# Kernel tuning notes

Measured on AMD Instinct MI355X. Metric: run time of the kernel, lower is better.

Reference implementation:

```python
import jax, jax.numpy as jnp
import numpy as np

B, D, K, E = 4096, 2048, 512, 8  # tokens, model dim, kept SVD rank, experts


def setup_inputs() -> dict:
    key = jax.random.key(0)
    ks = jax.random.split(key, 7)
    x = jax.random.normal(ks[0], (B, D), dtype=jnp.float32)
    # frozen base weight (stands in for pretrained_weight)
    W = jax.random.normal(ks[1], (D, D), dtype=jnp.float32) / np.sqrt(D)
    # frozen truncated SVD factors: U_k (D,K) left vecs, V_k (K,D) as sliced in the torch code
    U_k = jnp.linalg.qr(jax.random.normal(ks[2], (D, K), dtype=jnp.float32))[0]
    V_k = jnp.linalg.qr(jax.random.normal(ks[3], (D, K), dtype=jnp.float32))[0].T
    lambda_k = jax.random.normal(ks[4], (E, K), dtype=jnp.float32) * 0.02
    v = jnp.zeros((D,), dtype=jnp.float32)
    router_W1 = jax.random.normal(ks[5], (K, 1), dtype=jnp.float32)
    router_W2 = jax.random.normal(ks[6], (1, E), dtype=jnp.float32)
    return {"x": x, "W": W, "U_k": U_k, "V_k": V_k, "lambda_k": lambda_k,
            "v": v, "router_W1": router_W1, "router_W2": router_W2}


def reference(x, W, U_k, V_k, lambda_k, v, router_W1, router_W2):
    # routing: x @ U_k -> rank-1 router -> softmax over experts
    routing = x @ U_k                                   # (B,K)
    g = jax.nn.softmax((routing @ router_W1) @ router_W2, axis=-1)  # (B,E)
    # per-expert low-rank delta weight, materialized as in the original
    delta_W = jnp.einsum('dk,ek,kn->edn', U_k, lambda_k, V_k)       # (E,D,D)
    W_tot = W[None] + delta_W                           # (E,D,D)
    # F.linear semantics: out = x @ W_tot^T per expert
    expert_out = jnp.einsum('bd,end->ben', x, W_tot)    # (B,E,D)
    out = jnp.einsum('ben,be->bn', expert_out, g)       # gated combine
    return out * (1.0 + v)
```

## Files before the change

kernel.cpp:

```cpp
#include <hip/hip_runtime.h>
#include <hip/hip_bf16.h>
#include <cstdint>

#define B_TOK 4096
#define DDIM  2048
#define KR    512
#define NE    8

using f32x4  = __attribute__((ext_vector_type(4))) float;
using short8 = __attribute__((ext_vector_type(8))) short;
using u16 = unsigned short;

__device__ inline u16 f2bf(float f) {
    union { float f; uint32_t u; } x; x.f = f;
    uint32_t u = x.u;
    return (u16)((u + 0x7fffu + ((u >> 16) & 1u)) >> 16);
}
__device__ inline float bf2f(u16 h) {
    union { uint32_t u; float f; } x; x.u = ((uint32_t)h) << 16;
    return x.f;
}

__device__ inline void gload_lds16(const u16* g, u16* l) {
    __builtin_amdgcn_global_load_lds(
        (const __attribute__((address_space(1))) void*)g,
        (__attribute__((address_space(3))) void*)l, 16, 0, 0);
}

template<int COLS4, int SRC_LD, int DST_LD>
__device__ inline void cvt_region(const float* __restrict__ src,
                                  u16* __restrict__ dst, int i) {
    int r = i / COLS4, c = i - r * COLS4;
    float4 val = *((const float4*)(src + (size_t)r * SRC_LD) + c);
    ushort4 o;
    o.x = f2bf(val.x); o.y = f2bf(val.y); o.z = f2bf(val.z); o.w = f2bf(val.w);
    *(ushort4*)(dst + (size_t)r * DST_LD + c * 4) = o;
}

__global__ __launch_bounds__(256)
void prep_all(const float* __restrict__ x, const float* __restrict__ W,
              const float* __restrict__ U, const float* __restrict__ V,
              const float* __restrict__ W1,
              u16* __restrict__ Aaug, u16* __restrict__ BigB,
              u16* __restrict__ Vb) {
    constexpr int NB_COPY = 1792;
    constexpr int N_X = 4096 * 512;
    constexpr int N_W = 2048 * 512;
    constexpr int N_U = 2048 * 128;
    constexpr int N_V = 512 * 512;
    constexpr int N_Z = 63 * 512;
    constexpr int N_TOT = N_X + N_W + N_U + N_V + N_Z;
    int b = blockIdx.x;
    if (b < NB_COPY) {
        for (int i = b * 256 + threadIdx.x; i < N_TOT; i += NB_COPY * 256) {
            if (i < N_X)                cvt_region<512, 2048, 2560>(x, Aaug, i);
            else if (i < N_X + N_W)     cvt_region<512, 2048, 2560>(W, BigB, i - N_X);
            else if (i < N_X + N_W + N_U)
                cvt_region<128, 512, 2560>(U, BigB + 2048, i - N_X - N_W);
            else if (i < N_X + N_W + N_U + N_V)
                cvt_region<512, 2048, 2048>(V, Vb, i - N_X - N_W - N_U);
            else {
                int z = i - (N_X + N_W + N_U + N_V);
                ushort4 zz; zz.x = 0; zz.y = 0; zz.z = 0; zz.w = 0;
                *(ushort4*)(Vb + (size_t)513 * 2048 + (size_t)z * 4) = zz;
            }
        }
    } else {
        int wrow = (b - NB_COPY) * 4 + (threadIdx.x >> 6);
        int lane = threadIdx.x & 63;
        const float* row = U + (size_t)wrow * KR;
        float s = 0.f;
        #pragma unroll
        for (int k = 0; k < KR; k += 64) s += row[k + lane] * W1[k + lane];
        #pragma unroll
        for (int o = 32; o > 0; o >>= 1) s += __shfl_down(s, o);
        if (lane == 0) Vb[(size_t)512 * 2048 + wrow] = f2bf(s);
    }
}

__global__ __launch_bounds__(256)
void router3(const u16* __restrict__ tb, const float* __restrict__ W2,
             const float* __restrict__ lam, u16* __restrict__ Am) {
    int row = blockIdx.x, tid = threadIdx.x;
    const u16* tr = tb + (size_t)row * 576;
    float s = bf2f(tr[512]);

    float g[NE]; float mx = -1e30f;
    #pragma unroll
    for (int e = 0; e < NE; e++) { g[e] = s * W2[e]; mx = fmaxf(mx, g[e]); }
    float den = 0.f;
    #pragma unroll
    for (int e = 0; e < NE; e++) { g[e] = expf(g[e] - mx); den += g[e]; }
    float inv = 1.0f / den;

    #pragma unroll
    for (int kk = tid; kk < KR; kk += 256) {
        float mu = 0.f;
        #pragma unroll
        for (int e = 0; e < NE; e++) mu += g[e] * lam[e * KR + kk];
        Am[(size_t)row * 2560 + 2048 + kk] = f2bf(mu * inv * bf2f(tr[kk]));
    }
}

template<int BM, int BN, int WGM, int WGN, bool HAS_V, bool OUT_BF16>
__global__ __launch_bounds__(256, 2)
void gemm_db(const u16* __restrict__ A, const u16* __restrict__ Bm,
             void* __restrict__ Cv, const float* __restrict__ v,
             int N, int Kc, int lda, int ldb, int nbx) {
    constexpr int MF = BM / (WGM * 16);
    constexpr int NF = BN / (WGN * 16);
    constexpr int ISSA = BM / 32;
    constexpr int ISSB = BN / 32;
    __shared__ u16 sA[2 * BM * 64];
    __shared__ u16 sB[2 * BN * 64];

    const int tid = threadIdx.x;
    const int wid = tid >> 6, lane = tid & 63;
    const int l15 = lane & 15, l4 = lane >> 4;
    const int wm = wid / WGN, wn = wid % WGN;

    const int nwg = gridDim.x;
    const int id = (blockIdx.x & 7) * (nwg >> 3) + (blockIdx.x >> 3);
    const int row0 = (id / nbx) * BM;
    const int col0 = (id % nbx) * BN;

    const int srow = tid >> 3;
    const int scol = ((tid & 7) ^ (srow & 7)) << 3;
    const u16* gA = A + (size_t)(row0 + srow) * lda + scol;
    const u16* gB = Bm + (size_t)(col0 + srow) * ldb + scol;

    f32x4 acc[MF][NF] = {};
    const int nt = Kc >> 6;

    #pragma unroll
    for (int i = 0; i < ISSA; i++)
        gload_lds16(gA + (size_t)i * 32 * lda, sA + i * 2048 + wid * 512);
    #pragma unroll
    for (int i = 0; i < ISSB; i++)
        gload_lds16(gB + (size_t)i * 32 * ldb, sB + i * 2048 + wid * 512);
    __syncthreads();

    for (int t = 0; t < nt; ++t) {
        const int cur = t & 1;
        if (t + 1 < nt) {
            const int nxt = cur ^ 1;
            const u16* gAk = gA + (size_t)(t + 1) * 64;
            const u16* gBk = gB + (size_t)(t + 1) * 64;
            #pragma unroll
            for (int i = 0; i < ISSA; i++)
                gload_lds16(gAk + (size_t)i * 32 * lda,
                            sA + nxt * BM * 64 + i * 2048 + wid * 512);
            #pragma unroll
            for (int i = 0; i < ISSB; i++)
                gload_lds16(gBk + (size_t)i * 32 * ldb,
                            sB + nxt * BN * 64 + i * 2048 + wid * 512);
        }
        const u16* a0 = sA + cur * BM * 64;
        const u16* b0 = sB + cur * BN * 64;
        #pragma unroll
        for (int kc = 0; kc < 8; kc += 4) {
            short8 af[MF], bv[NF];
            #pragma unroll
            for (int mf = 0; mf < MF; mf++) {
                int row = wm * MF * 16 + mf * 16 + l15;
                int ch = (kc + l4) ^ (row & 7);
                af[mf] = *(const short8*)(a0 + row * 64 + ch * 8);
            }
            #pragma unroll
            for (int nf = 0; nf < NF; nf++) {
                int row = wn * NF * 16 + nf * 16 + l15;
                int ch = (kc + l4) ^ (row & 7);
                bv[nf] = *(const short8*)(b0 + row * 64 + ch * 8);
            }
            #pragma unroll
            for (int mf = 0; mf < MF; mf++)
                #pragma unroll
                for (int nf = 0; nf < NF; nf++)
                    acc[mf][nf] = __builtin_amdgcn_mfma_f32_16x16x32_bf16(
                        af[mf], bv[nf], acc[mf][nf], 0, 0, 0);
        }
        __syncthreads();
    }

    #pragma unroll
    for (int nf = 0; nf < NF; nf++) {
        int col = col0 + wn * NF * 16 + nf * 16 + l15;
        float sc = HAS_V ? (1.0f + v[col]) : 1.0f;
        #pragma unroll
        for (int mf = 0; mf < MF; mf++) {
            int row = row0 + wm * MF * 16 + mf * 16 + l4 * 4;
            #pragma unroll
            for (int r2 = 0; r2 < 4; r2++) {
                float val = acc[mf][nf][r2] * sc;
                if constexpr (OUT_BF16)
                    ((u16*)Cv)[(size_t)(row + r2) * N + col] = f2bf(val);
                else
                    ((float*)Cv)[(size_t)(row + r2) * N + col] = val;
            }
        }
    }
}

template<bool HAS_V, bool REGION>
__global__ __launch_bounds__(512, 1)
void gemm_ring(const u16* __restrict__ A, const u16* __restrict__ Bm,
               float* __restrict__ C, const float* __restrict__ v,
               int N, int Kc, int lda, int ldb, int nbx) {
    constexpr int BM = 256, BN = 128, WGN = 2;
    constexpr int MF = 4, NF = 4;
    constexpr int SLOT = (BM + BN) * 64;
    constexpr int ROWS = 64;
    constexpr int ISSA = 4, ISSB = 2;
    __shared__ u16 lds[3 * SLOT];

    const int tid = threadIdx.x;
    const int wid = tid >> 6, lane = tid & 63;
    const int l15 = lane & 15, l4 = lane >> 4;
    const int wm = wid / WGN, wn = wid % WGN;

    int row0, col0;
    if (REGION) {
        const int xcd = blockIdx.x & 7;
        const int j = blockIdx.x >> 3;
        row0 = ((xcd >> 1) * 4 + (j >> 3)) * BM;
        col0 = ((xcd & 1) * 8 + (j & 7)) * BN;
    } else {
        const int nwg = gridDim.x;
        const int id = (blockIdx.x & 7) * (nwg >> 3) + (blockIdx.x >> 3);
        row0 = (id / nbx) * BM;
        col0 = (id % nbx) * BN;
    }

    const int srow = tid >> 3;
    const int scol = ((tid & 7) ^ (srow & 7)) << 3;
    const u16* gA = A + (size_t)(row0 + srow) * lda + scol;
    const u16* gB = Bm + (size_t)(col0 + srow) * ldb + scol;

    f32x4 acc[MF][NF] = {};
    const int nt = Kc >> 6;

    #pragma unroll
    for (int p = 0; p < 2; p++) {
        const u16* gAt = gA + p * 64;
        const u16* gBt = gB + p * 64;
        u16* sl = lds + p * SLOT;
        #pragma unroll
        for (int i = 0; i < ISSA; i++)
            gload_lds16(gAt + (size_t)i * ROWS * lda,
                        sl + i * ROWS * 64 + wid * 512);
        #pragma unroll
        for (int i = 0; i < ISSB; i++)
            gload_lds16(gBt + (size_t)i * ROWS * ldb,
                        sl + BM * 64 + i * ROWS * 64 + wid * 512);
    }
    asm volatile("s_waitcnt vmcnt(6)" ::: "memory");
    __builtin_amdgcn_s_barrier();
    asm volatile("" ::: "memory");

    int sc = 0, sp = 2;
    for (int t = 0; t < nt; ++t) {
        if (t + 2 < nt) {
            const u16* gAt = gA + (size_t)(t + 2) * 64;
            const u16* gBt = gB + (size_t)(t + 2) * 64;
            u16* sl = lds + sp * SLOT;
            #pragma unroll
            for (int i = 0; i < ISSA; i++)
                gload_lds16(gAt + (size_t)i * ROWS * lda,
                            sl + i * ROWS * 64 + wid * 512);
            #pragma unroll
            for (int i = 0; i < ISSB; i++)
                gload_lds16(gBt + (size_t)i * ROWS * ldb,
                            sl + BM * 64 + i * ROWS * 64 + wid * 512);
        }
        const u16* a0 = lds + sc * SLOT;
        const u16* b0 = a0 + BM * 64;
        __builtin_amdgcn_s_setprio(1);
        #pragma unroll
        for (int kc = 0; kc < 8; kc += 4) {
            short8 af[MF], bv[NF];
            #pragma unroll
            for (int mf = 0; mf < MF; mf++) {
                int row = wm * MF * 16 + mf * 16 + l15;
                int ch = (kc + l4) ^ (row & 7);
                af[mf] = *(const short8*)(a0 + row * 64 + ch * 8);
            }
            #pragma unroll
            for (int nf = 0; nf < NF; nf++) {
                int row = wn * NF * 16 + nf * 16 + l15;
                int ch = (kc + l4) ^ (row & 7);
                bv[nf] = *(const short8*)(b0 + row * 64 + ch * 8);
            }
            #pragma unroll
            for (int mf = 0; mf < MF; mf++)
                #pragma unroll
                for (int nf = 0; nf < NF; nf++)
                    acc[mf][nf] = __builtin_amdgcn_mfma_f32_16x16x32_bf16(
                        af[mf], bv[nf], acc[mf][nf], 0, 0, 0);
        }
        __builtin_amdgcn_s_setprio(0);

        const int rem = nt - 1 - t;
        if (rem == 0) break;
        if (rem >= 2) asm volatile("s_waitcnt vmcnt(6)" ::: "memory");
        else          asm volatile("s_waitcnt vmcnt(0)" ::: "memory");
        __builtin_amdgcn_s_barrier();
        asm volatile("" ::: "memory");
        sc = (sc == 2) ? 0 : sc + 1;
        sp = (sp == 2) ? 0 : sp + 1;
    }

    #pragma unroll
    for (int nf = 0; nf < NF; nf++) {
        int col = col0 + wn * NF * 16 + nf * 16 + l15;
        float sc2 = HAS_V ? (1.0f + v[col]) : 1.0f;
        #pragma unroll
        for (int mf = 0; mf < MF; mf++) {
            int row = row0 + wm * MF * 16 + mf * 16 + l4 * 4;
            #pragma unroll
            for (int r2 = 0; r2 < 4; r2++)
                C[(size_t)(row + r2) * N + col] = acc[mf][nf][r2] * sc2;
        }
    }
}

extern "C" void kernel_launch(void* const* d_in, const int* in_sizes, int n_in,
                              void* d_out, int out_size, void* d_ws, size_t ws_size,
                              hipStream_t stream) {
    const float* x   = (const float*)d_in[0];
    const float* W   = (const float*)d_in[1];
    const float* U   = (const float*)d_in[2];
    const float* V   = (const float*)d_in[3];
    const float* lam = (const float*)d_in[4];
    const float* v   = (const float*)d_in[5];
    const float* W1  = (const float*)d_in[6];
    const float* W2  = (const float*)d_in[7];
    float* out = (float*)d_out;

    char* ws = (char*)d_ws;
    u16* Aaug  = (u16*)ws;
    u16* BigB  = (u16*)(ws + 20971520);
    u16* Vb    = (u16*)(ws + 31457280);
    u16* tmatb = (u16*)(ws + 33816576);

    prep_all<<<2304, 256, 0, stream>>>(x, W, U, V, W1, Aaug, BigB, Vb);

    gemm_db<128, 64, 4, 1, false, true><<<288, 256, 0, stream>>>(
        Aaug, Vb, tmatb, nullptr, 576, 2048, 2560, 2048, 9);

    router3<<<4096, 256, 0, stream>>>(tmatb, W2, lam, Aaug);

    gemm_ring<true, true><<<256, 512, 0, stream>>>(
        Aaug, BigB, out, v, 2048, 2560, 2560, 2560, 16);
}
```

Baseline: 99.55 us.

## Overlap W/U bf16 conversion with routing GEMM via extra blocks; precompute LDS offsets

The fp32-to-bf16 conversion of W and U moves out of the prep kernel into 256 extra blocks appended to the routing GEMM launch, so this conversion runs alongside the small GEMM instead of serialising before it. Prep shrinks to x and V conversion with fewer blocks. The main ring GEMM also precomputes swizzled LDS offsets once per thread instead of recomputing them every k-tile. This adds register pressure in the ring kernel and relies on the extra blocks not slowing the GEMM blocks they share the device with.

```diff
diff --git a/kernel.cpp b/kernel.cpp
--- a/kernel.cpp
+++ b/kernel.cpp
@@ -38,29 +38,21 @@
 }
 
 __global__ __launch_bounds__(256)
-void prep_all(const float* __restrict__ x, const float* __restrict__ W,
-              const float* __restrict__ U, const float* __restrict__ V,
-              const float* __restrict__ W1,
-              u16* __restrict__ Aaug, u16* __restrict__ BigB,
-              u16* __restrict__ Vb) {
-    constexpr int NB_COPY = 1792;
+void prep_all(const float* __restrict__ x, const float* __restrict__ U,
+              const float* __restrict__ V, const float* __restrict__ W1,
+              u16* __restrict__ Aaug, u16* __restrict__ Vb) {
+    constexpr int NB_COPY = 1024;
     constexpr int N_X = 4096 * 512;
-    constexpr int N_W = 2048 * 512;
-    constexpr int N_U = 2048 * 128;
     constexpr int N_V = 512 * 512;
     constexpr int N_Z = 63 * 512;
-    constexpr int N_TOT = N_X + N_W + N_U + N_V + N_Z;
+    constexpr int N_TOT = N_X + N_V + N_Z;
     int b = blockIdx.x;
     if (b < NB_COPY) {
         for (int i = b * 256 + threadIdx.x; i < N_TOT; i += NB_COPY * 256) {
-            if (i < N_X)                cvt_region<512, 2048, 2560>(x, Aaug, i);
-            else if (i < N_X + N_W)     cvt_region<512, 2048, 2560>(W, BigB, i - N_X);
-            else if (i < N_X + N_W + N_U)
-                cvt_region<128, 512, 2560>(U, BigB + 2048, i - N_X - N_W);
-            else if (i < N_X + N_W + N_U + N_V)
-                cvt_region<512, 2048, 2048>(V, Vb, i - N_X - N_W - N_U);
+            if (i < N_X)            cvt_region<512, 2048, 2560>(x, Aaug, i);
+            else if (i < N_X + N_V) cvt_region<512, 2048, 2048>(V, Vb, i - N_X);
             else {
-                int z = i - (N_X + N_W + N_U + N_V);
+                int z = i - (N_X + N_V);
                 ushort4 zz; zz.x = 0; zz.y = 0; zz.z = 0; zz.w = 0;
                 *(ushort4*)(Vb + (size_t)513 * 2048 + (size_t)z * 4) = zz;
             }
@@ -102,10 +94,12 @@
     }
 }
 
-template<int BM, int BN, int WGM, int WGN, bool HAS_V, bool OUT_BF16>
+template<int BM, int BN, int WGM, int WGN, int NCOMP, bool OUT_BF16>
 __global__ __launch_bounds__(256, 2)
 void gemm_db(const u16* __restrict__ A, const u16* __restrict__ Bm,
-             void* __restrict__ Cv, const float* __restrict__ v,
+             void* __restrict__ Cv,
+             const float* __restrict__ Wsrc, const float* __restrict__ Usrc,
+             u16* __restrict__ BigB,
              int N, int Kc, int lda, int ldb, int nbx) {
     constexpr int MF = BM / (WGM * 16);
     constexpr int NF = BN / (WGN * 16);
@@ -114,13 +108,23 @@
     __shared__ u16 sA[2 * BM * 64];
     __shared__ u16 sB[2 * BN * 64];
 
+    if (blockIdx.x >= NCOMP) {
+        constexpr int N_W = 2048 * 512;
+        constexpr int N_U = 2048 * 128;
+        int cb = blockIdx.x - NCOMP;
+        for (int i = cb * 256 + threadIdx.x; i < N_W + N_U; i += 256 * 256) {
+            if (i < N_W) cvt_region<512, 2048, 2560>(Wsrc, BigB, i);
+            else         cvt_region<128, 512, 2560>(Usrc, BigB + 2048, i - N_W);
+        }
+        return;
+    }
+
     const int tid = threadIdx.x;
     const int wid = tid >> 6, lane = tid & 63;
     const int l15 = lane & 15, l4 = lane >> 4;
     const int wm = wid / WGN, wn = wid % WGN;
 
-    const int nwg = gridDim.x;
-    const int id = (blockIdx.x & 7) * (nwg >> 3) + (blockIdx.x >> 3);
+    const int id = ((int)blockIdx.x & 7) * (NCOMP >> 3) + ((int)blockIdx.x >> 3);
     const int row0 = (id / nbx) * BM;
     const int col0 = (id % nbx) * BN;
 
@@ -185,13 +189,12 @@
     #pragma unroll
     for (int nf = 0; nf < NF; nf++) {
         int col = col0 + wn * NF * 16 + nf * 16 + l15;
-        float sc = HAS_V ? (1.0f + v[col]) : 1.0f;
         #pragma unroll
         for (int mf = 0; mf < MF; mf++) {
             int row = row0 + wm * MF * 16 + mf * 16 + l4 * 4;
             #pragma unroll
             for (int r2 = 0; r2 < 4; r2++) {
-                float val = acc[mf][nf][r2] * sc;
+                float val = acc[mf][nf][r2];
                 if constexpr (OUT_BF16)
                     ((u16*)Cv)[(size_t)(row + r2) * N + col] = f2bf(val);
                 else
@@ -201,11 +204,11 @@
     }
 }
 
-template<bool HAS_V, bool REGION>
+template<bool HAS_V>
 __global__ __launch_bounds__(512, 1)
 void gemm_ring(const u16* __restrict__ A, const u16* __restrict__ Bm,
                float* __restrict__ C, const float* __restrict__ v,
-               int N, int Kc, int lda, int ldb, int nbx) {
+               int N, int Kc, int lda, int ldb) {
     constexpr int BM = 256, BN = 128, WGN = 2;
     constexpr int MF = 4, NF = 4;
     constexpr int SLOT = (BM + BN) * 64;
@@ -218,23 +221,30 @@
     const int l15 = lane & 15, l4 = lane >> 4;
     const int wm = wid / WGN, wn = wid % WGN;
 
-    int row0, col0;
-    if (REGION) {
-        const int xcd = blockIdx.x & 7;
-        const int j = blockIdx.x >> 3;
-        row0 = ((xcd >> 1) * 4 + (j >> 3)) * BM;
-        col0 = ((xcd & 1) * 8 + (j & 7)) * BN;
-    } else {
-        const int nwg = gridDim.x;
-        const int id = (blockIdx.x & 7) * (nwg >> 3) + (blockIdx.x >> 3);
-        row0 = (id / nbx) * BM;
-        col0 = (id % nbx) * BN;
-    }
+    const int xcd = blockIdx.x & 7;
+    const int j = blockIdx.x >> 3;
+    const int row0 = ((xcd >> 1) * 4 + (j >> 3)) * BM;
+    const int col0 = ((xcd & 1) * 8 + (j & 7)) * BN;
 
     const int srow = tid >> 3;
     const int scol = ((tid & 7) ^ (srow & 7)) << 3;
     const u16* gA = A + (size_t)(row0 + srow) * lda + scol;
     const u16* gB = Bm + (size_t)(col0 + srow) * ldb + scol;
+
+    int aoff[2][MF], boff[2][NF];
+    #pragma unroll
+    for (int kc = 0; kc < 2; kc++) {
+        #pragma unroll
+        for (int mf = 0; mf < MF; mf++) {
+            int row = wm * MF * 16 + mf * 16 + l15;
+            aoff[kc][mf] = row * 64 + (((kc * 4) + l4) ^ (row & 7)) * 8;
+        }
+        #pragma unroll
+        for (int nf = 0; nf < NF; nf++) {
+            int row = wn * NF * 16 + nf * 16 + l15;
+            boff[kc][nf] = BM * 64 + row * 64 + (((kc * 4) + l4) ^ (row & 7)) * 8;
+        }
+    }
 
     f32x4 acc[MF][NF] = {};
     const int nt = Kc >> 6;
@@ -272,24 +282,17 @@
                 gload_lds16(gBt + (size_t)i * ROWS * ldb,
                             sl + BM * 64 + i * ROWS * 64 + wid * 512);
         }
-        const u16* a0 = lds + sc * SLOT;
-        const u16* b0 = a0 + BM * 64;
+        const u16* s0 = lds + sc * SLOT;
         __builtin_amdgcn_s_setprio(1);
         #pragma unroll
-        for (int kc = 0; kc < 8; kc += 4) {
+        for (int kc = 0; kc < 2; kc++) {
             short8 af[MF], bv[NF];
             #pragma unroll
-            for (int mf = 0; mf < MF; mf++) {
-                int row = wm * MF * 16 + mf * 16 + l15;
-                int ch = (kc + l4) ^ (row & 7);
-                af[mf] = *(const short8*)(a0 + row * 64 + ch * 8);
-            }
-            #pragma unroll
-            for (int nf = 0; nf < NF; nf++) {
-                int row = wn * NF * 16 + nf * 16 + l15;
-                int ch = (kc + l4) ^ (row & 7);
-                bv[nf] = *(const short8*)(b0 + row * 64 + ch * 8);
-            }
+            for (int mf = 0; mf < MF; mf++)
+                af[mf] = *(const short8*)(s0 + aoff[kc][mf]);
+            #pragma unroll
+            for (int nf = 0; nf < NF; nf++)
+                bv[nf] = *(const short8*)(s0 + boff[kc][nf]);
             #pragma unroll
             for (int mf = 0; mf < MF; mf++)
                 #pragma unroll
@@ -342,13 +345,13 @@
     u16* Vb    = (u16*)(ws + 31457280);
     u16* tmatb = (u16*)(ws + 33816576);
 
-    prep_all<<<2304, 256, 0, stream>>>(x, W, U, V, W1, Aaug, BigB, Vb);
-
-    gemm_db<128, 64, 4, 1, false, true><<<288, 256, 0, stream>>>(
-        Aaug, Vb, tmatb, nullptr, 576, 2048, 2560, 2048, 9);
+    prep_all<<<1536, 256, 0, stream>>>(x, U, V, W1, Aaug, Vb);
+
+    gemm_db<128, 64, 4, 1, 288, true><<<544, 256, 0, stream>>>(
+        Aaug, Vb, tmatb, W, U, BigB, 576, 2048, 2560, 2048, 9);
 
     router3<<<4096, 256, 0, stream>>>(tmatb, W2, lam, Aaug);
 
-    gemm_ring<true, true><<<256, 512, 0, stream>>>(
-        Aaug, BigB, out, v, 2048, 2560, 2560, 2560, 16);
-}
+    gemm_ring<true><<<256, 512, 0, stream>>>(
+        Aaug, BigB, out, v, 2048, 2560, 2560, 2560);
+}
```

Measured after the change: 95.22 us. 1.05x faster.
